# Optimization experiments

Measured on AMD Instinct MI355X. Metric: run time of the kernel, lower is better.

## Reference

```python
import jax, jax.numpy as jnp
import numpy as np

B, S, D, H, DFF = 2, 2048, 1024, 16, 4096
DK = D // H
EPS = 1e-6
MASK_FILL = -1.0  # original code uses -1**9 == -1 (precedence bug), NOT -1e9


def layernorm(x, gamma, beta):
    # original: (x - mean) / (std + eps), std unbiased (torch default ddof=1), scalar gamma/beta
    mean = jnp.mean(x, axis=-1, keepdims=True)
    std = jnp.std(x, axis=-1, keepdims=True, ddof=1)
    return gamma * (x - mean) / (std + EPS) + beta


def setup_inputs() -> dict:
    key = jax.random.key(0)
    ks = jax.random.split(key, 12)
    sc = 0.02
    return {
        "x": jax.random.normal(ks[0], (B, S, D), jnp.float32),
        "src_mask": jnp.ones((B, 1, 1, S), jnp.int32),
        "wq": jax.random.normal(ks[1], (D, D), jnp.float32) * sc,
        "bq": jnp.zeros((D,), jnp.float32),
        "wk": jax.random.normal(ks[2], (D, D), jnp.float32) * sc,
        "bk": jnp.zeros((D,), jnp.float32),
        "wv": jax.random.normal(ks[3], (D, D), jnp.float32) * sc,
        "bv": jnp.zeros((D,), jnp.float32),
        "wo": jax.random.normal(ks[4], (D, D), jnp.float32) * sc,
        "bo": jnp.zeros((D,), jnp.float32),
        "w1": jax.random.normal(ks[5], (D, DFF), jnp.float32) * sc,
        "b1": jnp.zeros((DFF,), jnp.float32),
        "w2": jax.random.normal(ks[6], (DFF, D), jnp.float32) * sc,
        "b2": jnp.zeros((D,), jnp.float32),
        "g1": jnp.ones((), jnp.float32),
        "be1": jnp.zeros((), jnp.float32),
        "g2": jnp.ones((), jnp.float32),
        "be2": jnp.zeros((), jnp.float32),
    }


def reference(x, src_mask, wq, bq, wk, bk, wv, bv, wo, bo,
              w1, b1, w2, b2, g1, be1, g2, be2):
    # --- residual 1: pre-LN self-attention ---
    xn = layernorm(x, g1, be1)
    q = (xn @ wq + bq).reshape(B, S, H, DK).transpose(0, 2, 1, 3)  # [B,H,S,DK]
    k = (xn @ wk + bk).reshape(B, S, H, DK).transpose(0, 2, 1, 3)
    v = (xn @ wv + bv).reshape(B, S, H, DK).transpose(0, 2, 1, 3)
    scores = jnp.einsum('bhqd,bhkd->bhqk', q, k) / jnp.sqrt(jnp.float32(DK))
    scores = jnp.where(src_mask == 0, MASK_FILL, scores)
    attn = jax.nn.softmax(scores, axis=-1)
    ctx = jnp.einsum('bhqk,bhkd->bhqd', attn, v)
    ctx = ctx.transpose(0, 2, 1, 3).reshape(B, S, D)
    attn_out = ctx @ wo + bo
    x = x + attn_out  # dropout is identity in eval

    # --- residual 2: pre-LN feed-forward ---
    xn = layernorm(x, g2, be2)
    h = jax.nn.relu(xn @ w1 + b1)
    ff_out = h @ w2 + b2
    return x + ff_out
```

## Files before the change

### kernel.cpp

```cpp
#include <hip/hip_runtime.h>

typedef unsigned short u16;
typedef __bf16 bf16x8 __attribute__((ext_vector_type(8)));
typedef float f32x4 __attribute__((ext_vector_type(4)));

#define AS1U(p) ((__attribute__((address_space(1))) unsigned int*)(p))
#define AS3U(p) ((__attribute__((address_space(3))) unsigned int*)(p))

__device__ __forceinline__ u16 f2bf(float f) {
  union { float f; unsigned int i; } c; c.f = f;
  return (u16)((c.i + 0x7FFFu + ((c.i >> 16) & 1u)) >> 16);
}
__device__ __forceinline__ u16 f2bf_trunc(float f) {
  union { float f; unsigned int i; } c; c.f = f;
  return (u16)(c.i >> 16);
}

template <int BM, int BN, int BK, int OMODE>
__global__ __launch_bounds__(256) void gemm_bt(
    const u16* __restrict__ A, long lda,
    const u16* __restrict__ B, long ldb,
    void* __restrict__ Cv, long ldc,
    int K, float scale, const float* __restrict__ bias,
    const float* __restrict__ res, long ldres, int relu) {
  constexpr int WN = (BN == 128) ? 64 : 32;
  constexpr int MI = 4, NJ = WN / 16;
  constexpr int KK = BK / 32;
  __shared__ u16 As0[BM * BK], As1[BM * BK];
  __shared__ u16 Bs0[BN * BK], Bs1[BN * BK];
  const int t = threadIdx.x;
  const int w = t >> 6, l = t & 63;
  const int wr = w >> 1, wc = w & 1;
  const int quad = l >> 4, mlo = l & 15;
  const long row0 = (long)blockIdx.x * BM;
  const long col0 = (long)blockIdx.y * BN;

  f32x4 acc[MI][NJ] = {};

  auto stage = [&](u16 (&Ad)[BM * BK], u16 (&Bd)[BN * BK], int k0) {
    if (BK == 32) {
#pragma unroll
      for (int i = 0; i < BM / 64; i++) {
        int s = t + i * 256, r = s >> 2, c = s & 3;
        const u16* g = A + (row0 + r) * lda + k0 + c * 8;
        __builtin_amdgcn_global_load_lds(AS1U(g), AS3U(&Ad[s * 8]), 16, 0, 0);
      }
#pragma unroll
      for (int i = 0; i < BN / 64; i++) {
        int s = t + i * 256, r = s >> 2, c = s & 3;
        const u16* g = B + (col0 + r) * ldb + k0 + c * 8;
        __builtin_amdgcn_global_load_lds(AS1U(g), AS3U(&Bd[s * 8]), 16, 0, 0);
      }
    } else {
#pragma unroll
      for (int i = 0; i < BM / 32; i++) {
        int s = t + i * 256, r = s >> 3, c = s & 7;
        const u16* g = A + (row0 + r) * lda + k0 + (c ^ (r & 7)) * 8;
        __builtin_amdgcn_global_load_lds(AS1U(g), AS3U(&Ad[s * 8]), 16, 0, 0);
      }
#pragma unroll
      for (int i = 0; i < BN / 32; i++) {
        int s = t + i * 256, r = s >> 3, c = s & 7;
        const u16* g = B + (col0 + r) * ldb + k0 + (c ^ (r & 7)) * 8;
        __builtin_amdgcn_global_load_lds(AS1U(g), AS3U(&Bd[s * 8]), 16, 0, 0);
      }
    }
  };
  auto compute = [&](const u16 (&Asr)[BM * BK], const u16 (&Bsr)[BN * BK]) {
#pragma unroll
    for (int kk = 0; kk < KK; kk++) {
      bf16x8 a[MI], b[NJ];
#pragma unroll
      for (int i = 0; i < MI; i++) {
        int r = wr * 64 + i * 16 + mlo;
        a[i] = (BK == 32) ? *(const bf16x8*)&Asr[(r * 4 + quad) * 8]
                          : *(const bf16x8*)&Asr[(r * 8 + ((kk * 4 + quad) ^ (r & 7))) * 8];
      }
#pragma unroll
      for (int j = 0; j < NJ; j++) {
        int r = wc * WN + j * 16 + mlo;
        b[j] = (BK == 32) ? *(const bf16x8*)&Bsr[(r * 4 + quad) * 8]
                          : *(const bf16x8*)&Bsr[(r * 8 + ((kk * 4 + quad) ^ (r & 7))) * 8];
      }
#pragma unroll
      for (int i = 0; i < MI; i++)
#pragma unroll
        for (int j = 0; j < NJ; j++)
          acc[i][j] = __builtin_amdgcn_mfma_f32_16x16x32_bf16(a[i], b[j], acc[i][j], 0, 0, 0);
    }
  };

  stage(As0, Bs0, 0);
  for (int k0 = 0; k0 < K; k0 += 2 * BK) {
    __syncthreads();
    stage(As1, Bs1, k0 + BK);
    compute(As0, Bs0);
    __syncthreads();
    if (k0 + 2 * BK < K) stage(As0, Bs0, k0 + 2 * BK);
    compute(As1, Bs1);
  }

#pragma unroll
  for (int i = 0; i < MI; i++) {
#pragma unroll
    for (int j = 0; j < NJ; j++) {
      const long gn = col0 + wc * WN + j * 16 + mlo;
      const float bv = bias ? bias[gn] : 0.0f;
#pragma unroll
      for (int r = 0; r < 4; r++) {
        const long gm = row0 + wr * 64 + i * 16 + quad * 4 + r;
        float v = acc[i][j][r] * scale + bv;
        if (relu && v < 0.0f) v = 0.0f;
        if (res) v += res[gm * ldres + gn];
        if (OMODE == 0) ((float*)Cv)[gm * ldc + gn] = v;
        else ((u16*)Cv)[gm * ldc + gn] = f2bf(v);
      }
    }
  }
}

__global__ __launch_bounds__(256) void flash_attn(
    const u16* __restrict__ QKV, const u16* __restrict__ VT,
    const int* __restrict__ mask, u16* __restrict__ ctx) {
  __shared__ u16 Ks[2][64 * 64];
  __shared__ u16 Vs[2][64 * 64];
  __shared__ u16 Ps[128 * 64];
  const int t = threadIdx.x;
  const int w = t >> 6, l = t & 63;
  const int quad = l >> 4, mlo = l & 15;
  const int z = blockIdx.z, b = z >> 4, h = z & 15;
  const long q0 = (long)blockIdx.x * 128;
  const u16* Qg = QKV + (long)b * (2048L * 3072) + h * 64;
  const u16* Kg = Qg + 1024;
  const u16* Vg = VT + (long)b * (1024L * 2048) + (long)(h * 64) * 2048;
  const int* mrow = mask + b * 2048;

#pragma unroll
  for (int i = 0; i < 2; i++) {
    int s = t + i * 256, r = s >> 3, c = s & 7;
    __builtin_amdgcn_global_load_lds(AS1U(Kg + (long)r * 3072 + (c ^ (r & 7)) * 8),
                                     AS3U(&Ks[0][s * 8]), 16, 0, 0);
    __builtin_amdgcn_global_load_lds(AS1U(Vg + (long)r * 2048 + (c ^ (r & 7)) * 8),
                                     AS3U(&Vs[0][s * 8]), 16, 0, 0);
  }
  bf16x8 aq[2][2];
#pragma unroll
  for (int i = 0; i < 2; i++)
#pragma unroll
    for (int kk = 0; kk < 2; kk++) {
      const u16* g = Qg + (q0 + w * 32 + i * 16 + mlo) * 3072 + kk * 32 + quad * 8;
      union { uint4 u; bf16x8 v; } c; c.u = *(const uint4*)g;
      aq[i][kk] = c.v;
    }

  f32x4 o[2][5] = {};
  union { u16 s[8]; bf16x8 v; } ones;
#pragma unroll
  for (int e = 0; e < 8; e++) ones.s[e] = 0x3F80;
  const float CS = 0.125f * 1.44269504f;
  const float CM = -1.44269504f;

  for (int it = 0; it < 32; ++it) {
    const int cur = it & 1;
    const int key0 = it * 64;
    __syncthreads();
    if (it + 1 < 32) {
      const int nb = 1 - cur;
      const u16* Kg2 = Kg + (long)(it + 1) * 64 * 3072;
      const u16* Vg2 = Vg + (it + 1) * 64;
#pragma unroll
      for (int i2 = 0; i2 < 2; i2++) {
        int s = t + i2 * 256, r = s >> 3, c = s & 7;
        __builtin_amdgcn_global_load_lds(AS1U(Kg2 + (long)r * 3072 + (c ^ (r & 7)) * 8),
                                         AS3U(&Ks[nb][s * 8]), 16, 0, 0);
        __builtin_amdgcn_global_load_lds(AS1U(Vg2 + (long)r * 2048 + (c ^ (r & 7)) * 8),
                                         AS3U(&Vs[nb][s * 8]), 16, 0, 0);
      }
    }
    int mz[4];
#pragma unroll
    for (int j = 0; j < 4; j++) mz[j] = mrow[key0 + j * 16 + mlo];
    f32x4 sa[2][4] = {};
#pragma unroll
    for (int kk = 0; kk < 2; kk++) {
      bf16x8 bk[4];
#pragma unroll
      for (int j = 0; j < 4; j++) {
        int rr = j * 16 + mlo;
        bk[j] = *(const bf16x8*)&Ks[cur][(rr * 8 + ((kk * 4 + quad) ^ (mlo & 7))) * 8];
      }
#pragma unroll
      for (int i = 0; i < 2; i++)
#pragma unroll
        for (int j = 0; j < 4; j++)
          sa[i][j] = __builtin_amdgcn_mfma_f32_16x16x32_bf16(aq[i][kk], bk[j], sa[i][j], 0, 0, 0);
    }
#pragma unroll
    for (int i = 0; i < 2; i++) {
      const int rbase = w * 32 + i * 16 + quad * 4;
      const int skey = (rbase >> 2) & 7;
#pragma unroll
      for (int j = 0; j < 4; j++) {
        const int col = j * 16 + mlo;
        u16* pp = &Ps[rbase * 64 + (((col >> 3) ^ skey) << 3) + (col & 7)];
#pragma unroll
        for (int r = 0; r < 4; r++) {
          float s = (mz[j] == 0) ? CM : sa[i][j][r] * CS;
          pp[r * 64] = f2bf_trunc(__builtin_amdgcn_exp2f(s));
        }
      }
    }
#pragma unroll
    for (int kk = 0; kk < 2; kk++) {
      bf16x8 ap[2], bv[4];
#pragma unroll
      for (int i = 0; i < 2; i++) {
        const int row = w * 32 + i * 16 + mlo;
        const int skey = (row >> 2) & 7;
        ap[i] = *(const bf16x8*)&Ps[(row * 8 + ((kk * 4 + quad) ^ skey)) * 8];
      }
#pragma unroll
      for (int j = 0; j < 4; j++) {
        int rr = j * 16 + mlo;
        bv[j] = *(const bf16x8*)&Vs[cur][(rr * 8 + ((kk * 4 + quad) ^ (mlo & 7))) * 8];
      }
#pragma unroll
      for (int i = 0; i < 2; i++) {
#pragma unroll
        for (int j = 0; j < 4; j++)
          o[i][j] = __builtin_amdgcn_mfma_f32_16x16x32_bf16(ap[i], bv[j], o[i][j], 0, 0, 0);
        o[i][4] = __builtin_amdgcn_mfma_f32_16x16x32_bf16(ap[i], ones.v, o[i][4], 0, 0, 0);
      }
    }
  }
  u16* cb = ctx + (long)b * (2048L * 1024) + q0 * 1024 + h * 64;
#pragma unroll
  for (int i = 0; i < 2; i++)
#pragma unroll
    for (int r = 0; r < 4; r++) {
      float inv = 1.0f / o[i][4][r];
      int row = w * 32 + i * 16 + quad * 4 + r;
#pragma unroll
      for (int j = 0; j < 4; j++)
        cb[(long)row * 1024 + j * 16 + mlo] = f2bf(o[i][j][r] * inv);
    }
}

__device__ __forceinline__ void ln_row(const float* __restrict__ x, u16* __restrict__ y,
                                       const float* __restrict__ g, const float* __restrict__ b,
                                       long row, float* ss, float* s2) {
  const float* xr = x + row * 1024;
  float v[4];
  float s = 0.f, sq = 0.f;
#pragma unroll
  for (int i = 0; i < 4; i++) {
    float f = xr[threadIdx.x + i * 256];
    v[i] = f; s += f; sq += f * f;
  }
#pragma unroll
  for (int o = 32; o > 0; o >>= 1) { s += __shfl_xor(s, o, 64); sq += __shfl_xor(sq, o, 64); }
  const int w = threadIdx.x >> 6;
  if ((threadIdx.x & 63) == 0) { ss[w] = s; s2[w] = sq; }
  __syncthreads();
  s = ss[0] + ss[1] + ss[2] + ss[3];
  sq = s2[0] + s2[1] + s2[2] + s2[3];
  const float mean = s * (1.0f / 1024.0f);
  float var = (sq - s * mean) * (1.0f / 1023.0f);
  var = fmaxf(var, 0.0f);
  const float sc = g[0] / (sqrtf(var) + 1e-6f);
  const float be = b[0];
#pragma unroll
  for (int i = 0; i < 4; i++)
    y[row * 1024 + threadIdx.x + i * 256] = f2bf((v[i] - mean) * sc + be);
}

__global__ __launch_bounds__(256) void ln_kernel(const float* __restrict__ x, u16* __restrict__ y,
                                                 const float* __restrict__ g, const float* __restrict__ b) {
  __shared__ float ss[4], s2[4];
  ln_row(x, y, g, b, blockIdx.x, ss, s2);
}

__global__ __launch_bounds__(256) void prep_kernel(
    const float* __restrict__ x, const float* __restrict__ g1, const float* __restrict__ be1,
    const float* __restrict__ wq, const float* __restrict__ wk, const float* __restrict__ wv,
    const float* __restrict__ wo, const float* __restrict__ w1, const float* __restrict__ w2,
    const float* __restrict__ bq, const float* __restrict__ bk, const float* __restrict__ bv,
    u16* __restrict__ xnH, u16* __restrict__ WqkvT, u16* __restrict__ woT,
    u16* __restrict__ w1T, u16* __restrict__ w2T, float* __restrict__ biasQKV) {
  __shared__ float tile[32][33];
  __shared__ float ss[4], s2[4];
  const int bid = blockIdx.x;
  if (bid >= 12300) {
    ln_row(x, xnH, g1, be1, bid - 12300, ss, s2);
    return;
  }
  if (bid >= 12288) {
    const int i = (bid - 12288) * 256 + threadIdx.x;
    if (i < 3072) biasQKV[i] = (i < 1024) ? bq[i] : ((i < 2048) ? bk[i - 1024] : bv[i - 2048]);
    return;
  }
  const float* in; u16* out; long ldin, ldo; int ti, tiles_x;
  if (bid < 1024)      { in = wq; out = WqkvT;                     ldin = 1024; ldo = 1024; ti = bid;        tiles_x = 32; }
  else if (bid < 2048) { in = wk; out = WqkvT + (size_t)1024*1024; ldin = 1024; ldo = 1024; ti = bid - 1024; tiles_x = 32; }
  else if (bid < 3072) { in = wv; out = WqkvT + (size_t)2048*1024; ldin = 1024; ldo = 1024; ti = bid - 2048; tiles_x = 32; }
  else if (bid < 4096) { in = wo; out = woT;                       ldin = 1024; ldo = 1024; ti = bid - 3072; tiles_x = 32; }
  else if (bid < 8192) { in = w1; out = w1T;                       ldin = 4096; ldo = 1024; ti = bid - 4096; tiles_x = 128; }
  else                 { in = w2; out = w2T;                       ldin = 1024; ldo = 4096; ti = bid - 8192; tiles_x = 32; }
  const int bx = (ti % tiles_x) * 32, by = (ti / tiles_x) * 32;
  const int tx = threadIdx.x & 31, ty = threadIdx.x >> 5;
#pragma unroll
  for (int i = 0; i < 32; i += 8) tile[ty + i][tx] = in[(long)(by + ty + i) * ldin + bx + tx];
  __syncthreads();
#pragma unroll
  for (int i = 0; i < 32; i += 8)
    out[(long)(bx + ty + i) * ldo + by + tx] = f2bf(tile[tx][ty + i]);
}

__global__ __launch_bounds__(256) void ttrans1(const u16* __restrict__ in, long ldin, long siz,
                                               u16* __restrict__ out, long ldo, long soz) {
  __shared__ u16 tile[32][33];
  const long zi = (long)blockIdx.z * siz, zo = (long)blockIdx.z * soz;
  const int bx = blockIdx.x * 32, by = blockIdx.y * 32;
  const int tx = threadIdx.x & 31, ty = threadIdx.x >> 5;
#pragma unroll
  for (int i = 0; i < 32; i += 8)
    tile[ty + i][tx] = in[zi + (long)(by + ty + i) * ldin + bx + tx];
  __syncthreads();
#pragma unroll
  for (int i = 0; i < 32; i += 8)
    out[zo + (long)(bx + ty + i) * ldo + by + tx] = tile[tx][ty + i];
}

extern "C" void kernel_launch(void* const* d_in, const int* in_sizes, int n_in,
                              void* d_out, int out_size, void* d_ws, size_t ws_size,
                              hipStream_t stream) {
  const float* x   = (const float*)d_in[0];
  const int*   msk = (const int*)d_in[1];
  const float* wq  = (const float*)d_in[2];
  const float* bq  = (const float*)d_in[3];
  const float* wk  = (const float*)d_in[4];
  const float* bk  = (const float*)d_in[5];
  const float* wv  = (const float*)d_in[6];
  const float* bv  = (const float*)d_in[7];
  const float* wo  = (const float*)d_in[8];
  const float* bo  = (const float*)d_in[9];
  const float* w1  = (const float*)d_in[10];
  const float* b1  = (const float*)d_in[11];
  const float* w2  = (const float*)d_in[12];
  const float* b2  = (const float*)d_in[13];
  const float* g1  = (const float*)d_in[14];
  const float* be1 = (const float*)d_in[15];
  const float* g2  = (const float*)d_in[16];
  const float* be2 = (const float*)d_in[17];
  float* out = (float*)d_out;

  char* basep = (char*)d_ws;
  size_t off = 0;
  auto au = [&](size_t nelem) -> u16* {
    u16* r = (u16*)(basep + off);
    off += ((nelem * 2) + 255) & ~(size_t)255;
    return r;
  };
  auto afp = [&](size_t nelem) -> float* {
    float* r = (float*)(basep + off);
    off += ((nelem * 4) + 255) & ~(size_t)255;
    return r;
  };

  u16* xnH  = au((size_t)4096 * 1024);
  u16* QKV  = au((size_t)4096 * 3072);
  u16* VTH  = au((size_t)2 * 1024 * 2048);
  u16* ctxH = au((size_t)4096 * 1024);
  float* x1 = afp((size_t)4096 * 1024);
  u16* hb   = au((size_t)4096 * 4096);
  u16* WqkvT = au((size_t)3072 * 1024);
  u16* woT  = au((size_t)1024 * 1024);
  u16* w1T  = au((size_t)4096 * 1024);
  u16* w2T  = au((size_t)1024 * 4096);
  float* biasQKV = afp(3072);

  const dim3 blk(256);

  prep_kernel<<<16396, blk, 0, stream>>>(x, g1, be1, wq, wk, wv, wo, w1, w2,
                                         bq, bk, bv, xnH, WqkvT, woT, w1T, w2T, biasQKV);

  gemm_bt<128, 128, 32, 2><<<dim3(32, 24), blk, 0, stream>>>(
      xnH, 1024, WqkvT, 1024, QKV, 3072, 1024, 1.0f,
      biasQKV, (const float*)0, 0, 0);

  ttrans1<<<dim3(32, 64, 2), blk, 0, stream>>>(
      QKV + 2048, 3072, (long)2048 * 3072, VTH, 2048, (long)1024 * 2048);

  flash_attn<<<dim3(16, 1, 32), blk, 0, stream>>>(QKV, VTH, msk, ctxH);

  gemm_bt<128, 64, 64, 0><<<dim3(32, 16), blk, 0, stream>>>(
      ctxH, 1024, woT, 1024, x1, 1024, 1024, 1.0f, bo, x, 1024, 0);

  ln_kernel<<<4096, blk, 0, stream>>>(x1, xnH, g2, be2);

  gemm_bt<128, 128, 32, 2><<<dim3(32, 32), blk, 0, stream>>>(
      xnH, 1024, w1T, 1024, hb, 4096, 1024, 1.0f,
      b1, (const float*)0, 0, 1);

  gemm_bt<128, 64, 64, 0><<<dim3(32, 16), blk, 0, stream>>>(
      hb, 4096, w2T, 4096, out, 1024, 4096, 1.0f, b2, x1, 1024, 0);
}
```

Baseline: 368.2 us.

## Rewrite flash attention with 32x32 MFMA and in-register P via permlane swap

The attention kernel moves from 16x16x32 to 32x32x16 MFMA tiles and computes S transposed (K as the A operand). The probability tile then stays in registers and is reshaped with packed bf16 conversion and v_permlane32_swap instead of a round trip through the shared Ps buffer. The mask is read once per key block with a ballot, and an all-ones fast path skips per-element selects. It also adds s_setprio around the MFMA groups and raises launch bounds to two blocks per SU, trading register pressure (f32x16 accumulators) for less LDS traffic and fewer instructions.

Result: no change. 374.1 us (+1.6%).

```diff
diff --git a/kernel.cpp b/kernel.cpp
--- a/kernel.cpp
+++ b/kernel.cpp
@@ -3,6 +3,7 @@
 typedef unsigned short u16;
 typedef __bf16 bf16x8 __attribute__((ext_vector_type(8)));
 typedef float f32x4 __attribute__((ext_vector_type(4)));
+typedef float f32x16 __attribute__((ext_vector_type(16)));
 
 #define AS1U(p) ((__attribute__((address_space(1))) unsigned int*)(p))
 #define AS3U(p) ((__attribute__((address_space(3))) unsigned int*)(p))
@@ -14,6 +15,14 @@
 __device__ __forceinline__ u16 f2bf_trunc(float f) {
   union { float f; unsigned int i; } c; c.f = f;
   return (u16)(c.i >> 16);
+}
+__device__ __forceinline__ unsigned cvt_pk_bf16(float lo, float hi) {
+  unsigned r;
+  asm("v_cvt_pk_bf16_f32 %0, %1, %2" : "=v"(r) : "v"(lo), "v"(hi));
+  return r;
+}
+__device__ __forceinline__ void plswap(unsigned& a, unsigned& b) {
+  asm("v_permlane32_swap_b32 %0, %1" : "+v"(a), "+v"(b));
 }
 
 template <int BM, int BN, int BK, int OMODE>
@@ -119,15 +128,14 @@
   }
 }
 
-__global__ __launch_bounds__(256) void flash_attn(
+__global__ __launch_bounds__(256, 2) void flash_attn(
     const u16* __restrict__ QKV, const u16* __restrict__ VT,
     const int* __restrict__ mask, u16* __restrict__ ctx) {
   __shared__ u16 Ks[2][64 * 64];
   __shared__ u16 Vs[2][64 * 64];
-  __shared__ u16 Ps[128 * 64];
   const int t = threadIdx.x;
   const int w = t >> 6, l = t & 63;
-  const int quad = l >> 4, mlo = l & 15;
+  const int hi = l >> 5, lq = l & 31, rx = lq & 7;
   const int z = blockIdx.z, b = z >> 4, h = z & 15;
   const long q0 = (long)blockIdx.x * 128;
   const u16* Qg = QKV + (long)b * (2048L * 3072) + h * 64;
@@ -143,17 +151,16 @@
     __builtin_amdgcn_global_load_lds(AS1U(Vg + (long)r * 2048 + (c ^ (r & 7)) * 8),
                                      AS3U(&Vs[0][s * 8]), 16, 0, 0);
   }
-  bf16x8 aq[2][2];
-#pragma unroll
-  for (int i = 0; i < 2; i++)
-#pragma unroll
-    for (int kk = 0; kk < 2; kk++) {
-      const u16* g = Qg + (q0 + w * 32 + i * 16 + mlo) * 3072 + kk * 32 + quad * 8;
-      union { uint4 u; bf16x8 v; } c; c.u = *(const uint4*)g;
-      aq[i][kk] = c.v;
-    }
-
-  f32x4 o[2][5] = {};
+
+  bf16x8 aq[4];
+#pragma unroll
+  for (int kk = 0; kk < 4; kk++) {
+    const u16* g = Qg + (q0 + w * 32 + lq) * 3072 + kk * 16 + hi * 8;
+    union { uint4 u; bf16x8 v; } cc; cc.u = *(const uint4*)g;
+    aq[kk] = cc.v;
+  }
+
+  f32x16 o[2] = {}, den = {};
   union { u16 s[8]; bf16x8 v; } ones;
 #pragma unroll
   for (int e = 0; e < 8; e++) ones.s[e] = 0x3F80;
@@ -177,73 +184,70 @@
                                          AS3U(&Vs[nb][s * 8]), 16, 0, 0);
       }
     }
-    int mz[4];
-#pragma unroll
-    for (int j = 0; j < 4; j++) mz[j] = mrow[key0 + j * 16 + mlo];
-    f32x4 sa[2][4] = {};
-#pragma unroll
-    for (int kk = 0; kk < 2; kk++) {
-      bf16x8 bk[4];
-#pragma unroll
-      for (int j = 0; j < 4; j++) {
-        int rr = j * 16 + mlo;
-        bk[j] = *(const bf16x8*)&Ks[cur][(rr * 8 + ((kk * 4 + quad) ^ (mlo & 7))) * 8];
-      }
-#pragma unroll
-      for (int i = 0; i < 2; i++)
-#pragma unroll
-        for (int j = 0; j < 4; j++)
-          sa[i][j] = __builtin_amdgcn_mfma_f32_16x16x32_bf16(aq[i][kk], bk[j], sa[i][j], 0, 0, 0);
+    const unsigned long long bm = __ballot(mrow[key0 + l] != 0);
+    const bool allone = (bm == ~0ull);
+
+#pragma unroll
+    for (int kt = 0; kt < 2; kt++) {
+      f32x16 sa = {};
+      const int rk = kt * 32 + lq;
+      __builtin_amdgcn_s_setprio(1);
+#pragma unroll
+      for (int kk = 0; kk < 4; kk++) {
+        bf16x8 ak = *(const bf16x8*)&Ks[cur][(rk * 8 + ((2 * kk + hi) ^ rx)) * 8];
+        sa = __builtin_amdgcn_mfma_f32_32x32x16_bf16(ak, aq[kk], sa, 0, 0, 0);
+      }
+      __builtin_amdgcn_s_setprio(0);
+
+      float p[16];
+      if (allone) {
+#pragma unroll
+        for (int g = 0; g < 16; g++) p[g] = __builtin_amdgcn_exp2f(sa[g] * CS);
+      } else {
+#pragma unroll
+        for (int g = 0; g < 16; g++) {
+          const int k = kt * 32 + (g & 3) + 8 * (g >> 2) + 4 * hi;
+          const float s = ((bm >> k) & 1) ? sa[g] * CS : CM;
+          p[g] = __builtin_amdgcn_exp2f(s);
+        }
+      }
+      unsigned wd[4][2];
+#pragma unroll
+      for (int g = 0; g < 4; g++) {
+        wd[g][0] = cvt_pk_bf16(p[4 * g + 0], p[4 * g + 1]);
+        wd[g][1] = cvt_pk_bf16(p[4 * g + 2], p[4 * g + 3]);
+      }
+#pragma unroll
+      for (int c = 0; c < 2; c++) {
+        plswap(wd[2 * c][0], wd[2 * c + 1][0]);
+        plswap(wd[2 * c][1], wd[2 * c + 1][1]);
+        union { unsigned u[4]; bf16x8 v; } pa;
+        pa.u[0] = wd[2 * c][0];
+        pa.u[1] = wd[2 * c][1];
+        pa.u[2] = wd[2 * c + 1][0];
+        pa.u[3] = wd[2 * c + 1][1];
+        const int cg = kt * 2 + c;
+        __builtin_amdgcn_s_setprio(1);
+#pragma unroll
+        for (int dt = 0; dt < 2; dt++) {
+          const int rv = dt * 32 + lq;
+          bf16x8 bv = *(const bf16x8*)&Vs[cur][(rv * 8 + ((2 * cg + hi) ^ rx)) * 8];
+          o[dt] = __builtin_amdgcn_mfma_f32_32x32x16_bf16(pa.v, bv, o[dt], 0, 0, 0);
+        }
+        den = __builtin_amdgcn_mfma_f32_32x32x16_bf16(pa.v, ones.v, den, 0, 0, 0);
+        __builtin_amdgcn_s_setprio(0);
+      }
     }
-#pragma unroll
-    for (int i = 0; i < 2; i++) {
-      const int rbase = w * 32 + i * 16 + quad * 4;
-      const int skey = (rbase >> 2) & 7;
-#pragma unroll
-      for (int j = 0; j < 4; j++) {
-        const int col = j * 16 + mlo;
-        u16* pp = &Ps[rbase * 64 + (((col >> 3) ^ skey) << 3) + (col & 7)];
-#pragma unroll
-        for (int r = 0; r < 4; r++) {
-          float s = (mz[j] == 0) ? CM : sa[i][j][r] * CS;
-          pp[r * 64] = f2bf_trunc(__builtin_amdgcn_exp2f(s));
-        }
-      }
-    }
-#pragma unroll
-    for (int kk = 0; kk < 2; kk++) {
-      bf16x8 ap[2], bv[4];
-#pragma unroll
-      for (int i = 0; i < 2; i++) {
-        const int row = w * 32 + i * 16 + mlo;
-        const int skey = (row >> 2) & 7;
-        ap[i] = *(const bf16x8*)&Ps[(row * 8 + ((kk * 4 + quad) ^ skey)) * 8];
-      }
-#pragma unroll
-      for (int j = 0; j < 4; j++) {
-        int rr = j * 16 + mlo;
-        bv[j] = *(const bf16x8*)&Vs[cur][(rr * 8 + ((kk * 4 + quad) ^ (mlo & 7))) * 8];
-      }
-#pragma unroll
-      for (int i = 0; i < 2; i++) {
-#pragma unroll
-        for (int j = 0; j < 4; j++)
-          o[i][j] = __builtin_amdgcn_mfma_f32_16x16x32_bf16(ap[i], bv[j], o[i][j], 0, 0, 0);
-        o[i][4] = __builtin_amdgcn_mfma_f32_16x16x32_bf16(ap[i], ones.v, o[i][4], 0, 0, 0);
-      }
-    }
-  }
-  u16* cb = ctx + (long)b * (2048L * 1024) + q0 * 1024 + h * 64;
-#pragma unroll
-  for (int i = 0; i < 2; i++)
-#pragma unroll
-    for (int r = 0; r < 4; r++) {
-      float inv = 1.0f / o[i][4][r];
-      int row = w * 32 + i * 16 + quad * 4 + r;
-#pragma unroll
-      for (int j = 0; j < 4; j++)
-        cb[(long)row * 1024 + j * 16 + mlo] = f2bf(o[i][j][r] * inv);
-    }
+  }
+
+  u16* cb = ctx + (long)b * (2048L * 1024) + (q0 + w * 32) * 1024 + h * 64;
+#pragma unroll
+  for (int g = 0; g < 16; g++) {
+    const int row = (g & 3) + 8 * (g >> 2) + 4 * hi;
+    const float inv = 1.0f / den[g];
+    cb[(long)row * 1024 + lq] = f2bf(o[0][g] * inv);
+    cb[(long)row * 1024 + 32 + lq] = f2bf(o[1][g] * inv);
+  }
 }
 
 __device__ __forceinline__ void ln_row(const float* __restrict__ x, u16* __restrict__ y,
```
